# Optimization experiments

Measured on AMD Instinct MI355X. Metric: run time of the kernel, lower is better.

Reference implementation:

```python
import jax, jax.numpy as jnp
import numpy as np

# Static config matching init_kwargs
SPATIAL_SCALE = 0.25
SAMPLING_RATIO = 2
PH, PW = 7, 7
ALIGNED = True
CLOCKWISE = False


def setup_inputs() -> dict:
    key = jax.random.key(0)
    k_feat, k_b, k_c, k_wh, k_a = jax.random.split(key, 5)
    N, C, H, W = 2, 256, 256, 256
    n_rois = 1024
    feat = jax.random.normal(k_feat, (N, C, H, W), dtype=jnp.float32)
    # rois: (batch_idx, cx, cy, w, h, angle) in IMAGE coordinates (stride-4 map)
    b = jax.random.randint(k_b, (n_rois,), 0, N).astype(jnp.float32)
    ctr = jax.random.uniform(k_c, (n_rois, 2), minval=0.0, maxval=1024.0)
    wh = jax.random.uniform(k_wh, (n_rois, 2), minval=32.0, maxval=320.0)
    ang = jax.random.uniform(k_a, (n_rois,), minval=-np.pi, maxval=np.pi)
    rois = jnp.concatenate([b[:, None], ctr, wh, ang[:, None]], axis=1).astype(jnp.float32)
    return {"input": feat, "rois": rois}


def _roi_align_rotated(feat, rois):
    N, C, H, W = feat.shape
    b = rois[:, 0].astype(jnp.int32)
    off = 0.5 if ALIGNED else 0.0
    cx = rois[:, 1] * SPATIAL_SCALE - off
    cy = rois[:, 2] * SPATIAL_SCALE - off
    rw = rois[:, 3] * SPATIAL_SCALE
    rh = rois[:, 4] * SPATIAL_SCALE
    th = -rois[:, 5] if CLOCKWISE else rois[:, 5]
    if not ALIGNED:
        rw = jnp.maximum(rw, 1.0)
        rh = jnp.maximum(rh, 1.0)
    bin_h = rh / PH  # [n]
    bin_w = rw / PW
    gh = gw = SAMPLING_RATIO  # sampling_ratio > 0 -> static grid

    py = jnp.arange(PH, dtype=feat.dtype)
    px = jnp.arange(PW, dtype=feat.dtype)
    sy = (jnp.arange(gh, dtype=feat.dtype) + 0.5) / gh
    sx = (jnp.arange(gw, dtype=feat.dtype) + 0.5) / gw
    # roi-local sample coords: yy [n,PH,gh], xx [n,PW,gw]
    yy = (-rh / 2)[:, None, None] + (py[None, :, None] + sy[None, None, :]) * bin_h[:, None, None]
    xx = (-rw / 2)[:, None, None] + (px[None, :, None] + sx[None, None, :]) * bin_w[:, None, None]
    # broadcast to [n,PH,PW,gh,gw]
    yy5 = yy[:, :, None, :, None]
    xx5 = xx[:, None, :, None, :]
    cos = jnp.cos(th)[:, None, None, None, None]
    sin = jnp.sin(th)[:, None, None, None, None]
    cyb = cy[:, None, None, None, None]
    cxb = cx[:, None, None, None, None]
    # mmcv convention: y = yy*cos - xx*sin + cy ; x = yy*sin + xx*cos + cx
    y = yy5 * cos - xx5 * sin + cyb
    x = yy5 * sin + xx5 * cos + cxb

    valid = (y > -1.0) & (y < H) & (x > -1.0) & (x < W)
    y = jnp.maximum(y, 0.0)
    x = jnp.maximum(x, 0.0)
    yl = y.astype(jnp.int32)
    xl = x.astype(jnp.int32)
    condy = yl >= H - 1
    condx = xl >= W - 1
    yl = jnp.where(condy, H - 1, yl)
    xl = jnp.where(condx, W - 1, xl)
    yh = jnp.minimum(yl + 1, H - 1)
    xh = jnp.minimum(xl + 1, W - 1)
    y = jnp.where(condy, yl.astype(y.dtype), y)
    x = jnp.where(condx, xl.astype(x.dtype), x)
    ly = y - yl
    lx = x - xl
    hy = 1.0 - ly
    hx = 1.0 - lx

    b5 = b[:, None, None, None, None]

    def gather(yi, xi):
        # -> [n,PH,PW,gh,gw,C]
        return feat[b5, :, yi, xi]

    v = ((hy * hx)[..., None] * gather(yl, xl)
         + (hy * lx)[..., None] * gather(yl, xh)
         + (ly * hx)[..., None] * gather(yh, xl)
         + (ly * lx)[..., None] * gather(yh, xh))
    v = jnp.where(valid[..., None], v, 0.0)
    out = v.mean(axis=(3, 4))  # average over the gh*gw samples -> [n,PH,PW,C]
    return jnp.transpose(out, (0, 3, 1, 2))  # [n,C,PH,PW]


def reference(input, rois):
    return _roi_align_rotated(input, rois)
```

## Files before the change

kernel.cpp:

```cpp
#include <hip/hip_runtime.h>
#include <hip/hip_fp16.h>

#define SPATIAL_SCALE 0.25f
#define PH_ 7
#define PW_ 7
#define NBINS 49
#define NSAMP 196
#define C_ 256
#define H_ 256
#define W_ 256
#define HW_ (H_ * W_)

__global__ __launch_bounds__(256) void transpose_nchw_nhwc(
    const float* __restrict__ in, float* __restrict__ out) {
  __shared__ float tile[64 * 68];
  const int b  = blockIdx.z;
  const int p0 = blockIdx.x * 64;
  const int c0 = blockIdx.y * 64;
  const int t  = threadIdx.x;
  const int i  = t & 15;
  const int q  = t >> 4;

  const float* src = in + (size_t)b * C_ * HW_ + (size_t)(c0 + 4 * q) * HW_
                        + (p0 + 4 * i);
  const float4 r0 = *(const float4*)(src + 0 * HW_);
  const float4 r1 = *(const float4*)(src + 1 * HW_);
  const float4 r2 = *(const float4*)(src + 2 * HW_);
  const float4 r3 = *(const float4*)(src + 3 * HW_);

  float* tp = &tile[(4 * i) * 68 + 4 * q];
  *(float4*)(tp + 0 * 68) = make_float4(r0.x, r1.x, r2.x, r3.x);
  *(float4*)(tp + 1 * 68) = make_float4(r0.y, r1.y, r2.y, r3.y);
  *(float4*)(tp + 2 * 68) = make_float4(r0.z, r1.z, r2.z, r3.z);
  *(float4*)(tp + 3 * 68) = make_float4(r0.w, r1.w, r2.w, r3.w);
  __syncthreads();

  float* dst = out + (size_t)b * HW_ * C_ + (size_t)(p0 + q) * C_ + (c0 + 4 * i);
#pragma unroll
  for (int k = 0; k < 4; ++k) {
    const float4 v = *(const float4*)&tile[(16 * k + q) * 68 + 4 * i];
    *(float4*)(dst + (size_t)(16 * k) * C_) = v;
  }
}

__global__ __launch_bounds__(256, 3) void roi_align_rotated_nhwc(
    const float* __restrict__ feat, const float* __restrict__ rois,
    float* __restrict__ out) {
  __shared__ int     d_off[NSAMP];
  __shared__ __half2 d_w[NSAMP * 2];
  __shared__ float   res[NBINS * 256];

  const int r = blockIdx.x;
  const int t = threadIdx.x;

  if (t < NSAMP) {
    const float* rp = rois + r * 6;
    const int   b  = (int)rp[0];
    const float cx = rp[1] * SPATIAL_SCALE - 0.5f;
    const float cy = rp[2] * SPATIAL_SCALE - 0.5f;
    const float rw = rp[3] * SPATIAL_SCALE;
    const float rh = rp[4] * SPATIAL_SCALE;
    float sn, cs;
    sincosf(rp[5], &sn, &cs);
    const float bin_h = rh / (float)PH_;
    const float bin_w = rw / (float)PW_;

    const int bin = t >> 2;
    const int sub = t & 3;
    const int ph  = bin / 7;
    const int pw  = bin - ph * 7;
    const int iy  = sub >> 1;
    const int ix  = sub & 1;

    const float yy = -0.5f * rh + ((float)ph + ((float)iy + 0.5f) * 0.5f) * bin_h;
    const float xx = -0.5f * rw + ((float)pw + ((float)ix + 0.5f) * 0.5f) * bin_w;
    float y = yy * cs - xx * sn + cy;
    float x = yy * sn + xx * cs + cx;

    const bool valid = (y > -1.0f) && (y < (float)H_) &&
                       (x > -1.0f) && (x < (float)W_);
    y = fminf(fmaxf(y, 0.0f), (float)(H_ - 1));
    x = fminf(fmaxf(x, 0.0f), (float)(W_ - 1));
    const int yl = (int)y;
    const int xl = (int)x;
    const float ly = y - (float)yl, lx = x - (float)xl;
    const float hy = 1.0f - ly, hx = 1.0f - lx;
    float w11 = hy * hx, w12 = hy * lx, w21 = ly * hx, w22 = ly * lx;
    if (!valid) { w11 = w12 = w21 = w22 = 0.0f; }

    const int base = ((b * H_ + yl) * W_ + xl) * C_;
    const int dxf  = (xl < W_ - 1) ? 1 : 0;
    const int dyf  = (yl < H_ - 1) ? 2 : 0;
    d_off[t]       = base | dxf | dyf;
    d_w[2 * t]     = __floats2half2_rn(w11, w12);
    d_w[2 * t + 1] = __floats2half2_rn(w21, w22);
  }
  __syncthreads();

  const int c = t;
  for (int bin = 0; bin < NBINS; ++bin) {
    float acc = 0.0f;
#pragma unroll
    for (int sub = 0; sub < 4; ++sub) {
      const int s    = bin * 4 + sub;
      const int pc   = d_off[s];
      const int base = (pc & ~255) + c;
      const int dx   = (pc & 1) ? C_ : 0;
      const int dy   = (pc & 2) ? (W_ * C_) : 0;
      const float2 wa = __half22float2(d_w[2 * s]);
      const float2 wb = __half22float2(d_w[2 * s + 1]);
      acc += wa.x * feat[base];
      acc += wa.y * feat[base + dx];
      acc += wb.x * feat[base + dy];
      acc += wb.y * feat[base + dx + dy];
    }
    res[bin * 256 + (c ^ (bin & 31))] = acc * 0.25f;
  }
  __syncthreads();

  float* outr = out + (size_t)r * (C_ * NBINS);
#pragma unroll 1
  for (int i = t; i < C_ * NBINS; i += 256) {
    const int cc = i / NBINS;
    const int bb = i - cc * NBINS;
    outr[i] = res[bb * 256 + (cc ^ (bb & 31))];
  }
}

__global__ __launch_bounds__(256) void roi_align_rotated_nchw(
    const float* __restrict__ feat, const float* __restrict__ rois,
    float* __restrict__ out) {
  __shared__ int   d_pix[NSAMP];
  __shared__ int   d_step[NSAMP];
  __shared__ float4 d_wt[NSAMP];
  __shared__ float res[NBINS * 257];

  const int r = blockIdx.x;
  const int t = threadIdx.x;
  if (t < NSAMP) {
    const float* rp = rois + r * 6;
    const int   b  = (int)rp[0];
    const float cx = rp[1] * SPATIAL_SCALE - 0.5f;
    const float cy = rp[2] * SPATIAL_SCALE - 0.5f;
    const float rw = rp[3] * SPATIAL_SCALE;
    const float rh = rp[4] * SPATIAL_SCALE;
    float sn, cs;
    sincosf(rp[5], &sn, &cs);
    const float bin_h = rh / (float)PH_;
    const float bin_w = rw / (float)PW_;
    const int bin = t >> 2, sub = t & 3;
    const int ph = bin / 7, pw = bin - ph * 7;
    const int iy = sub >> 1, ix = sub & 1;
    const float yy = -0.5f * rh + ((float)ph + ((float)iy + 0.5f) * 0.5f) * bin_h;
    const float xx = -0.5f * rw + ((float)pw + ((float)ix + 0.5f) * 0.5f) * bin_w;
    float y = yy * cs - xx * sn + cy;
    float x = yy * sn + xx * cs + cx;
    const bool valid = (y > -1.0f) && (y < (float)H_) &&
                       (x > -1.0f) && (x < (float)W_);
    y = fminf(fmaxf(y, 0.0f), (float)(H_ - 1));
    x = fminf(fmaxf(x, 0.0f), (float)(W_ - 1));
    const int yl = (int)y, xl = (int)x;
    const float ly = y - (float)yl, lx = x - (float)xl;
    const float hy = 1.0f - ly, hx = 1.0f - lx;
    float w11 = hy * hx, w12 = hy * lx, w21 = ly * hx, w22 = ly * lx;
    if (!valid) { w11 = w12 = w21 = w22 = 0.0f; }
    d_pix[t]  = (b * H_ + yl) * W_ + xl;
    d_step[t] = ((xl < W_ - 1) ? 1 : 0) | ((yl < H_ - 1) ? 2 : 0);
    d_wt[t]   = make_float4(w11, w12, w21, w22);
  }
  __syncthreads();

  const int c = t;
  const size_t coff = (size_t)c * HW_;
  for (int bin = 0; bin < NBINS; ++bin) {
    float acc = 0.0f;
#pragma unroll
    for (int sub = 0; sub < 4; ++sub) {
      const int s = bin * 4 + sub;
      const int p = d_pix[s];
      const int st = d_step[s];
      const int dx = (st & 1) ? 1 : 0;
      const int dy = (st & 2) ? W_ : 0;
      const float4 w = d_wt[s];
      const int bb = (p / HW_) * C_ * HW_ + (p % HW_);
      acc += w.x * feat[bb + coff];
      acc += w.y * feat[bb + coff + dx];
      acc += w.z * feat[bb + coff + dy];
      acc += w.w * feat[bb + coff + dx + dy];
    }
    res[bin * 257 + c] = acc * 0.25f;
  }
  __syncthreads();
  float* outr = out + (size_t)r * (C_ * NBINS);
#pragma unroll 1
  for (int i = t; i < C_ * NBINS; i += 256) {
    const int cc = i / NBINS;
    const int bb = i - cc * NBINS;
    outr[i] = res[bb * 257 + cc];
  }
}

extern "C" void kernel_launch(void* const* d_in, const int* in_sizes, int n_in,
                              void* d_out, int out_size, void* d_ws, size_t ws_size,
                              hipStream_t stream) {
  const float* feat = (const float*)d_in[0];
  const float* rois = (const float*)d_in[1];
  float* out = (float*)d_out;
  const int n_rois  = in_sizes[1] / 6;
  const int n_batch = in_sizes[0] / (C_ * HW_);

  const size_t need = (size_t)n_batch * C_ * HW_ * sizeof(float);
  if (ws_size >= need) {
    float* feat_t = (float*)d_ws;
    dim3 tg(HW_ / 64, C_ / 64, n_batch);
    hipLaunchKernelGGL(transpose_nchw_nhwc, tg, dim3(256), 0, stream, feat, feat_t);
    hipLaunchKernelGGL(roi_align_rotated_nhwc, dim3(n_rois), dim3(256),
                       0, stream, feat_t, rois, out);
  } else {
    hipLaunchKernelGGL(roi_align_rotated_nchw, dim3(n_rois), dim3(256),
                       0, stream, feat, rois, out);
  }
}
```

Before: 323.1 us.

## Store transposed feature map in fp16 and drop shared-memory output staging

The NHWC transpose now writes the feature map as half precision, which halves both the workspace write and the gather traffic in the ROI kernel. Each thread in the ROI kernel handles two channels through half2 loads and covers half of the bins, and interpolation weights are kept in fp32. The shared-memory result buffer and its transpose pass are removed, so each thread writes its outputs directly. This lowers shared-memory use so more blocks can be resident, but the direct writes are strided by bin and less coalesced, and rounding features to fp16 adds error.

```diff
diff --git a/kernel.cpp b/kernel.cpp
--- a/kernel.cpp
+++ b/kernel.cpp
@@ -11,8 +11,10 @@
 #define W_ 256
 #define HW_ (H_ * W_)
 
-__global__ __launch_bounds__(256) void transpose_nchw_nhwc(
-    const float* __restrict__ in, float* __restrict__ out) {
+struct H4 { __half2 a, b; };
+
+__global__ __launch_bounds__(256) void transpose_nchw_nhwc_h(
+    const float* __restrict__ in, __half* __restrict__ out) {
   __shared__ float tile[64 * 68];
   const int b  = blockIdx.z;
   const int p0 = blockIdx.x * 64;
@@ -35,20 +37,22 @@
   *(float4*)(tp + 3 * 68) = make_float4(r0.w, r1.w, r2.w, r3.w);
   __syncthreads();
 
-  float* dst = out + (size_t)b * HW_ * C_ + (size_t)(p0 + q) * C_ + (c0 + 4 * i);
+  __half* dst = out + (size_t)b * HW_ * C_ + (size_t)(p0 + q) * C_ + (c0 + 4 * i);
 #pragma unroll
   for (int k = 0; k < 4; ++k) {
     const float4 v = *(const float4*)&tile[(16 * k + q) * 68 + 4 * i];
-    *(float4*)(dst + (size_t)(16 * k) * C_) = v;
-  }
-}
-
-__global__ __launch_bounds__(256, 3) void roi_align_rotated_nhwc(
-    const float* __restrict__ feat, const float* __restrict__ rois,
+    H4 h;
+    h.a = __floats2half2_rn(v.x, v.y);
+    h.b = __floats2half2_rn(v.z, v.w);
+    *(H4*)(dst + (size_t)(16 * k) * C_) = h;
+  }
+}
+
+__global__ __launch_bounds__(256, 4) void roi_align_rotated_nhwc_h(
+    const __half* __restrict__ feat, const float* __restrict__ rois,
     float* __restrict__ out) {
-  __shared__ int     d_off[NSAMP];
-  __shared__ __half2 d_w[NSAMP * 2];
-  __shared__ float   res[NBINS * 256];
+  __shared__ int    d_off[NSAMP];
+  __shared__ float4 d_wt[NSAMP];
 
   const int r = blockIdx.x;
   const int t = threadIdx.x;
@@ -91,49 +95,47 @@
     const int base = ((b * H_ + yl) * W_ + xl) * C_;
     const int dxf  = (xl < W_ - 1) ? 1 : 0;
     const int dyf  = (yl < H_ - 1) ? 2 : 0;
-    d_off[t]       = base | dxf | dyf;
-    d_w[2 * t]     = __floats2half2_rn(w11, w12);
-    d_w[2 * t + 1] = __floats2half2_rn(w21, w22);
-  }
-  __syncthreads();
-
-  const int c = t;
-  for (int bin = 0; bin < NBINS; ++bin) {
-    float acc = 0.0f;
+    d_off[t] = base | dxf | dyf;
+    d_wt[t]  = make_float4(w11, w12, w21, w22);
+  }
+  __syncthreads();
+
+  const int c2   = t & 127;
+  const int bh   = t >> 7;
+  const int bin0 = bh ? 25 : 0;
+  const int bin1 = bh ? 49 : 25;
+  const int cb   = 2 * c2;
+  float* outr = out + (size_t)r * (C_ * NBINS) + (size_t)cb * NBINS;
+
+  for (int bin = bin0; bin < bin1; ++bin) {
+    float accx = 0.0f, accy = 0.0f;
 #pragma unroll
     for (int sub = 0; sub < 4; ++sub) {
-      const int s    = bin * 4 + sub;
-      const int pc   = d_off[s];
-      const int base = (pc & ~255) + c;
+      const int s  = bin * 4 + sub;
+      const int pc = d_off[s];
+      const float4 wt = d_wt[s];
+      const int base = (pc & ~255) + cb;
       const int dx   = (pc & 1) ? C_ : 0;
       const int dy   = (pc & 2) ? (W_ * C_) : 0;
-      const float2 wa = __half22float2(d_w[2 * s]);
-      const float2 wb = __half22float2(d_w[2 * s + 1]);
-      acc += wa.x * feat[base];
-      acc += wa.y * feat[base + dx];
-      acc += wb.x * feat[base + dy];
-      acc += wb.y * feat[base + dx + dy];
+      const float2 f00 = __half22float2(*(const __half2*)(feat + base));
+      const float2 f01 = __half22float2(*(const __half2*)(feat + base + dx));
+      const float2 f10 = __half22float2(*(const __half2*)(feat + base + dy));
+      const float2 f11 = __half22float2(*(const __half2*)(feat + base + dx + dy));
+      accx += wt.x * f00.x + wt.y * f01.x + wt.z * f10.x + wt.w * f11.x;
+      accy += wt.x * f00.y + wt.y * f01.y + wt.z * f10.y + wt.w * f11.y;
     }
-    res[bin * 256 + (c ^ (bin & 31))] = acc * 0.25f;
-  }
-  __syncthreads();
-
-  float* outr = out + (size_t)r * (C_ * NBINS);
-#pragma unroll 1
-  for (int i = t; i < C_ * NBINS; i += 256) {
-    const int cc = i / NBINS;
-    const int bb = i - cc * NBINS;
-    outr[i] = res[bb * 256 + (cc ^ (bb & 31))];
+    outr[bin]         = accx * 0.25f;
+    outr[NBINS + bin] = accy * 0.25f;
   }
 }
 
 __global__ __launch_bounds__(256) void roi_align_rotated_nchw(
     const float* __restrict__ feat, const float* __restrict__ rois,
     float* __restrict__ out) {
-  __shared__ int   d_pix[NSAMP];
-  __shared__ int   d_step[NSAMP];
+  __shared__ int    d_pix[NSAMP];
+  __shared__ int    d_step[NSAMP];
   __shared__ float4 d_wt[NSAMP];
-  __shared__ float res[NBINS * 257];
+  __shared__ float  res[NBINS * 257];
 
   const int r = blockIdx.x;
   const int t = threadIdx.x;
@@ -209,13 +211,13 @@
   const int n_rois  = in_sizes[1] / 6;
   const int n_batch = in_sizes[0] / (C_ * HW_);
 
-  const size_t need = (size_t)n_batch * C_ * HW_ * sizeof(float);
+  const size_t need = (size_t)n_batch * C_ * HW_ * sizeof(__half);
   if (ws_size >= need) {
-    float* feat_t = (float*)d_ws;
+    __half* feat_h = (__half*)d_ws;
     dim3 tg(HW_ / 64, C_ / 64, n_batch);
-    hipLaunchKernelGGL(transpose_nchw_nhwc, tg, dim3(256), 0, stream, feat, feat_t);
-    hipLaunchKernelGGL(roi_align_rotated_nhwc, dim3(n_rois), dim3(256),
-                       0, stream, feat_t, rois, out);
+    hipLaunchKernelGGL(transpose_nchw_nhwc_h, tg, dim3(256), 0, stream, feat, feat_h);
+    hipLaunchKernelGGL(roi_align_rotated_nhwc_h, dim3(n_rois), dim3(256),
+                       0, stream, feat_h, rois, out);
   } else {
     hipLaunchKernelGGL(roi_align_rotated_nchw, dim3(n_rois), dim3(256),
                        0, stream, feat, rois, out);
```

Result: slower. 350.2 us (+8.4%).
